# Optimization experiments

Hardware: AMD Instinct MI355X
Metric: run time of the kernel (lower is better)

The kernel has to match this reference:

```python
import jax, jax.numpy as jnp
import numpy as np

HID = 256
SLOTS = 64
K = 2
TAU = 8.0
EPS = 1e-5


def setup_inputs() -> dict:
    key = jax.random.key(0)
    ks = jax.random.split(key, 8)
    B, T = 512, 256
    s = lambda fan_in: 1.0 / np.sqrt(fan_in)
    return {
        "x": jax.random.uniform(ks[0], (B, T, 1), jnp.float32, 0.0, 10.0),
        "W_embed": jax.random.uniform(ks[1], (HID, 1), jnp.float32, -1.0, 1.0),
        "b_embed": jax.random.uniform(ks[2], (HID,), jnp.float32, -1.0, 1.0),
        "W_update": jax.random.uniform(ks[3], (HID, HID), jnp.float32, -s(HID), s(HID)),
        "b_update": jax.random.uniform(ks[4], (HID,), jnp.float32, -s(HID), s(HID)),
        "gamma": jnp.ones((HID,), jnp.float32),
        "beta": jnp.zeros((HID,), jnp.float32),
        "W_out": jax.random.uniform(ks[5], (10, HID), jnp.float32, -s(HID), s(HID)),
        "b_out": jax.random.uniform(ks[6], (10,), jnp.float32, -s(HID), s(HID)),
        "context_strength": jnp.float32(0.2),
    }


def _gaussian_attention(pointer, num_positions):
    # pointer: [B] float. Returns indices [B,5] int32, weights [B,5] float.
    offsets = jnp.arange(-K, K + 1)
    base = jnp.clip(jnp.floor(pointer).astype(jnp.int32), 0, num_positions - 1)
    indices = (base[:, None] + offsets[None, :]) % num_positions
    delta = indices.astype(pointer.dtype) - pointer[:, None]
    weights = jax.nn.softmax(-(delta ** 2) / TAU, axis=1)
    return indices, weights


def reference(x, W_embed, b_embed, W_update, b_update, gamma, beta, W_out, b_out, context_strength):
    B, T, _ = x.shape
    cs = jax.nn.sigmoid(context_strength)

    def step(carry, x_t):
        h, memory, pointer = carry  # [B,H], [B,SLOTS,H], [B]
        inp = jnp.tanh(x_t @ W_embed.T + b_embed)           # [B,H]
        indices, weights = _gaussian_attention(pointer, SLOTS)
        neighborhood = jnp.take_along_axis(memory, indices[:, :, None], axis=1)  # [B,5,H]
        context = jnp.einsum('bk,bkh->bh', weights, neighborhood)
        combined = inp + cs * context
        h = jnp.tanh((combined + h) @ W_update.T + b_update)
        mu = jnp.mean(h, axis=-1, keepdims=True)
        var = jnp.mean((h - mu) ** 2, axis=-1, keepdims=True)
        h = (h - mu) * jax.lax.rsqrt(var + EPS) * gamma + beta
        contribution = weights[:, :, None] * h[:, None, :]   # [B,5,H]
        memory = jax.vmap(lambda m, i, c: m.at[i].add(c))(memory, indices, contribution)
        pointer = (pointer + 1.0) % SLOTS
        return (h, memory, pointer), None

    h0 = jnp.zeros((B, HID), x.dtype)
    mem0 = jnp.zeros((B, SLOTS, HID), x.dtype)
    ptr0 = jnp.zeros((B,), x.dtype)
    (h, _, _), _ = jax.lax.scan(step, (h0, mem0, ptr0), jnp.swapaxes(x, 0, 1))
    return h @ W_out.T + b_out
```

## Files before the change

kernel.cpp:

```cpp
#include <hip/hip_runtime.h>


#define TT 256

typedef __bf16 bf16x8 __attribute__((ext_vector_type(8)));
typedef float  f32x4  __attribute__((ext_vector_type(4)));

__device__ __forceinline__ float fast_tanh(float x) {
    float e = __expf(2.f * x);
    return 1.f - __fdividef(2.f, e + 1.f);
}

template<int CTRL, int RM>
__device__ __forceinline__ float dpp_add(float v) {
    int t = __builtin_amdgcn_update_dpp(0, __float_as_int(v), CTRL, RM, 0xf, true);
    return v + __int_as_float(t);
}
template<int IMM>
__device__ __forceinline__ float swz_add(float v) {
    int t = __builtin_amdgcn_ds_swizzle(__float_as_int(v), IMM);
    return v + __int_as_float(t);
}

#define SMEM_BYTES 136528

__global__ __launch_bounds__(512, 2)
void postnorm_kernel(const float* __restrict__ x,
                     const float* __restrict__ W_embed,
                     const float* __restrict__ b_embed,
                     const float* __restrict__ W_update,
                     const float* __restrict__ b_update,
                     const float* __restrict__ gamma,
                     const float* __restrict__ beta,
                     const float* __restrict__ W_out,
                     const float* __restrict__ b_out,
                     const float* __restrict__ ctx_s,
                     float* __restrict__ out)
{
    extern __shared__ __align__(16) char smem[];
    float*  s_mem  = (float*)(smem);
    float*  s_x    = (float*)(smem + 131072);
    __bf16* s_v    = (__bf16*)(smem + 133120);
    float*  s_red1 = (float*)(smem + 134272);
    float*  s_red2 = (float*)(smem + 134336);
    float*  s_wt   = (float*)(smem + 134400);
    float*  s_oacc = (float*)(smem + 136448);

    const int tid  = threadIdx.x;
    const int wave = tid >> 6;
    const int lane = tid & 63;
    const int bn   = lane & 15;
    const int quad = lane >> 4;
    const int r0   = blockIdx.x * 2;

    const int b     = bn >> 1;
    const int row   = bn & 1;
    const int i_own = wave * 32 + (b >> 2) * 16 + quad * 4 + (b & 3);

    {   f32x4 z = {0.f, 0.f, 0.f, 0.f};
        f32x4* p = (f32x4*)s_mem;
        #pragma unroll
        for (int k = 0; k < 16; ++k) p[tid + k * 512] = z;
    }
    s_x[tid] = x[(r0 + (tid >> 8)) * TT + (tid & 255)];
    if (tid < 20) s_oacc[tid] = 0.f;

    if (tid < 64) {
        float wv[5]; float ssum = 0.f;
        #pragma unroll
        for (int k = 0; k < 5; ++k) {
            int idx = (tid + k - 2) & 63;
            float d = (float)idx - (float)tid;
            wv[k] = expf(-(d * d) * 0.125f);
            ssum += wv[k];
        }
        #pragma unroll
        for (int k = 0; k < 5; ++k) s_wt[tid * 8 + k] = wv[k] / ssum;
    }

    const float we  = W_embed[i_own];
    const float be  = b_embed[i_own];
    const float bu  = b_update[i_own];
    const float gm  = gamma[i_own];
    const float btt = beta[i_own];
    const float csv = 1.f / (1.f + expf(-ctx_s[0]));

    bf16x8 wfa[2][8];
    #pragma unroll
    for (int mt = 0; mt < 2; ++mt) {
        #pragma unroll
        for (int kt = 0; kt < 8; ++kt) {
            const float* wp = W_update + (wave * 32 + mt * 16 + bn) * 256
                                       + kt * 32 + quad * 8;
            f32x4 a = *(const f32x4*)wp;
            f32x4 bb = *(const f32x4*)(wp + 4);
            bf16x8 f;
            f[0] = (__bf16)a[0];  f[1] = (__bf16)a[1];
            f[2] = (__bf16)a[2];  f[3] = (__bf16)a[3];
            f[4] = (__bf16)bb[0]; f[5] = (__bf16)bb[1];
            f[6] = (__bf16)bb[2]; f[7] = (__bf16)bb[3];
            wfa[mt][kt] = f;
        }
    }

    __syncthreads();
    {
        float inp0 = fast_tanh(s_x[row * 256] * we + be);
        s_v[row * 288 + i_own] = (__bf16)inp0;
    }

    float wt0, wt1, wt2, wt3, wt4;
    {   f32x4 wv = *(const f32x4*)(s_wt);
        wt0 = wv[0]; wt1 = wv[1]; wt2 = wv[2]; wt3 = wv[3]; wt4 = s_wt[4];
    }
    f32x4 nw  = *(const f32x4*)(s_wt + 8);
    float nw4 = s_wt[8 + 4];
    float xn  = s_x[row * 256 + 1];
    float nf  = 0.f;
    __syncthreads();

    float hn = 0.f;
    float w0 = 0.f, w1 = 0.f, w2 = 0.f, w3 = 0.f, w4 = 0.f;
    float* mcol = s_mem + (row << 14) + i_own;
    const __bf16* vsrc = s_v + row * 288 + quad * 8;

    #pragma unroll 1
    for (int t = 0; t < TT; ++t) {
        float inp = fast_tanh(xn * we + be);

        f32x4 a0a = {0,0,0,0}, a0b = {0,0,0,0}, a1a = {0,0,0,0}, a1b = {0,0,0,0};
        #pragma unroll
        for (int kt = 0; kt < 4; ++kt) {
            bf16x8 bfr0 = *(const bf16x8*)(vsrc + kt * 32);
            bf16x8 bfr1 = *(const bf16x8*)(vsrc + (kt + 4) * 32);
            a0a = __builtin_amdgcn_mfma_f32_16x16x32_bf16(wfa[0][kt],     bfr0, a0a, 0, 0, 0);
            a1a = __builtin_amdgcn_mfma_f32_16x16x32_bf16(wfa[1][kt],     bfr0, a1a, 0, 0, 0);
            a0b = __builtin_amdgcn_mfma_f32_16x16x32_bf16(wfa[0][kt + 4], bfr1, a0b, 0, 0, 0);
            a1b = __builtin_amdgcn_mfma_f32_16x16x32_bf16(wfa[1][kt + 4], bfr1, a1b, 0, 0, 0);
        }

        f32x4 y0 = a0a + a0b, y1 = a1a + a1b;
        f32x4 ym = (b & 4) ? y1 : y0;
        float yA = (b & 2) ? ym[2] : ym[0];
        float yB = (b & 2) ? ym[3] : ym[1];
        float ysel = (b & 1) ? yB : yA;

        float yt = fast_tanh(ysel + bu);
        float s1 = yt, s2 = yt * yt;
        s1 = dpp_add<0x4E, 0xf>(s1);  s2 = dpp_add<0x4E, 0xf>(s2);
        s1 = swz_add<0x101F>(s1);     s2 = swz_add<0x101F>(s2);
        s1 = swz_add<0x201F>(s1);     s2 = swz_add<0x201F>(s2);
        s1 = swz_add<0x401F>(s1);     s2 = swz_add<0x401F>(s2);
        s1 += __shfl_xor(s1, 32, 64); s2 += __shfl_xor(s2, 32, 64);
        if (lane < 2) {
            s_red1[lane * 8 + wave] = s1;
            s_red2[lane * 8 + wave] = s2;
        }
        __syncthreads();

        f32x4 r1a = *(const f32x4*)(s_red1 + row * 8);
        f32x4 r1b = *(const f32x4*)(s_red1 + row * 8 + 4);
        f32x4 r2a = *(const f32x4*)(s_red2 + row * 8);
        f32x4 r2b = *(const f32x4*)(s_red2 + row * 8 + 4);
        float S1 = ((r1a[0] + r1a[1]) + (r1a[2] + r1a[3]))
                 + ((r1b[0] + r1b[1]) + (r1b[2] + r1b[3]));
        float S2 = ((r2a[0] + r2a[1]) + (r2a[2] + r2a[3]))
                 + ((r2b[0] + r2b[1]) + (r2b[2] + r2b[3]));
        float mu   = S1 * (1.f / 256.f);
        float var  = S2 * (1.f / 256.f) - mu * mu;
        float rstd = rsqrtf(var + 1e-5f);
        hn = (yt - mu) * rstd * gm + btt;

        w0 += wt0 * hn; w1 += wt1 * hn; w2 += wt2 * hn;
        w3 += wt3 * hn; w4 += wt4 * hn;

        mcol[((t - 2) & 63) << 8] = w0;
        w0 = w1; w1 = w2; w2 = w3; w3 = w4; w4 = nf;
        float ctx = ((nw[0] * w0 + nw[1] * w1) + (nw[2] * w2 + nw[3] * w3))
                  + nw4 * w4;
        float v = inp + csv * ctx + hn;
        s_v[row * 288 + i_own] = (__bf16)v;
        wt0 = nw[0]; wt1 = nw[1]; wt2 = nw[2]; wt3 = nw[3]; wt4 = nw4;

        nf  = mcol[((t + 4) & 63) << 8];
        {   const float* wp = s_wt + ((t + 2) & 63) * 8;
            nw  = *(const f32x4*)wp;
            nw4 = wp[4];
        }
        xn  = s_x[row * 256 + ((t + 2) & 255)];
        __syncthreads();
    }

    s_x[row * 256 + i_own] = hn;
    __syncthreads();
    {
        const int n = tid >> 8, i = tid & 255;
        float h = s_x[tid];
        #pragma unroll
        for (int o = 0; o < 10; ++o) {
            float p = h * W_out[o * 256 + i];
            #pragma unroll
            for (int m = 32; m >= 1; m >>= 1) p += __shfl_xor(p, m, 64);
            if (lane == 0) atomicAdd(&s_oacc[n * 10 + o], p);
        }
    }
    __syncthreads();
    if (tid < 20) {
        int nn = tid / 10, o = tid % 10;
        out[(r0 + nn) * 10 + o] = s_oacc[tid] + b_out[o];
    }
}

extern "C" void kernel_launch(void* const* d_in, const int* in_sizes, int n_in,
                              void* d_out, int out_size, void* d_ws, size_t ws_size,
                              hipStream_t stream) {
    const float* x    = (const float*)d_in[0];
    const float* W_e  = (const float*)d_in[1];
    const float* b_e  = (const float*)d_in[2];
    const float* W_u  = (const float*)d_in[3];
    const float* b_u  = (const float*)d_in[4];
    const float* gmm  = (const float*)d_in[5];
    const float* bta  = (const float*)d_in[6];
    const float* W_o  = (const float*)d_in[7];
    const float* b_o  = (const float*)d_in[8];
    const float* cst  = (const float*)d_in[9];
    float* out = (float*)d_out;

    (void)hipFuncSetAttribute(reinterpret_cast<const void*>(postnorm_kernel),
                              hipFuncAttributeMaxDynamicSharedMemorySize,
                              SMEM_BYTES);

    postnorm_kernel<<<dim3(256), dim3(512), SMEM_BYTES, stream>>>(
        x, W_e, b_e, W_u, b_u, gmm, bta, W_o, b_o, cst, out);
}
```

Baseline: 310.7 us.

## Fold LayerNorm into the matmul to drop one barrier per timestep

The recurrence is restructured algebraically. The raw tanh output (scaled by gamma) goes into the MFMA as a second operand column, and the LayerNorm mean and rstd are applied afterward as scalar corrections, using a precomputed W·gamma vector (yG) and a DPP exchange between paired lanes. This removes the mid-step barrier between the reduction and the next matvec. The reduction and s_v buffers are double-buffered, so each step needs only one __syncthreads, at the cost of doubling the N columns used in the MFMA and some added bf16 rounding error on the unnormalized values.

```diff
diff --git a/kernel.cpp b/kernel.cpp
--- a/kernel.cpp
+++ b/kernel.cpp
@@ -21,8 +21,12 @@
     int t = __builtin_amdgcn_ds_swizzle(__float_as_int(v), IMM);
     return v + __int_as_float(t);
 }
-
-#define SMEM_BYTES 136528
+__device__ __forceinline__ float dpp_xor2_mov(float v) {
+    int t = __builtin_amdgcn_update_dpp(0, __float_as_int(v), 0x4E, 0xf, 0xf, true);
+    return __int_as_float(t);
+}
+
+#define SMEM_BYTES 139856
 
 __global__ __launch_bounds__(512, 2)
 void postnorm_kernel(const float* __restrict__ x,
@@ -41,10 +45,10 @@
     float*  s_mem  = (float*)(smem);
     float*  s_x    = (float*)(smem + 131072);
     __bf16* s_v    = (__bf16*)(smem + 133120);
-    float*  s_red1 = (float*)(smem + 134272);
-    float*  s_red2 = (float*)(smem + 134336);
-    float*  s_wt   = (float*)(smem + 134400);
-    float*  s_oacc = (float*)(smem + 136448);
+    float*  s_red1 = (float*)(smem + 137472);
+    float*  s_red2 = (float*)(smem + 137600);
+    float*  s_wt   = (float*)(smem + 137728);
+    float*  s_oacc = (float*)(smem + 139776);
 
     const int tid  = threadIdx.x;
     const int wave = tid >> 6;
@@ -53,9 +57,12 @@
     const int quad = lane >> 4;
     const int r0   = blockIdx.x * 2;
 
-    const int b     = bn >> 1;
-    const int row   = bn & 1;
-    const int i_own = wave * 32 + (b >> 2) * 16 + quad * 4 + (b & 3);
+    const int row  = bn & 1;
+    const int pq   = (bn >> 1) & 1;
+    const int rep  = bn >> 2;
+    const int mt   = rep >> 1;
+    const int rsel = (rep & 1) * 2 + pq;
+    const int i_own = wave * 32 + mt * 16 + quad * 4 + rsel;
 
     {   f32x4 z = {0.f, 0.f, 0.f, 0.f};
         f32x4* p = (f32x4*)s_mem;
@@ -63,6 +70,7 @@
         for (int k = 0; k < 16; ++k) p[tid + k * 512] = z;
     }
     s_x[tid] = x[(r0 + (tid >> 8)) * TT + (tid & 255)];
+    if (tid < 64) ((float*)(smem + 137472))[tid] = 0.f;
     if (tid < 20) s_oacc[tid] = 0.f;
 
     if (tid < 64) {
@@ -87,10 +95,10 @@
 
     bf16x8 wfa[2][8];
     #pragma unroll
-    for (int mt = 0; mt < 2; ++mt) {
+    for (int mtt = 0; mtt < 2; ++mtt) {
         #pragma unroll
         for (int kt = 0; kt < 8; ++kt) {
-            const float* wp = W_update + (wave * 32 + mt * 16 + bn) * 256
+            const float* wp = W_update + (wave * 32 + mtt * 16 + bn) * 256
                                        + kt * 32 + quad * 8;
             f32x4 a = *(const f32x4*)wp;
             f32x4 bb = *(const f32x4*)(wp + 4);
@@ -99,35 +107,17 @@
             f[2] = (__bf16)a[2];  f[3] = (__bf16)a[3];
             f[4] = (__bf16)bb[0]; f[5] = (__bf16)bb[1];
             f[6] = (__bf16)bb[2]; f[7] = (__bf16)bb[3];
-            wfa[mt][kt] = f;
-        }
-    }
-
-    __syncthreads();
-    {
-        float inp0 = fast_tanh(s_x[row * 256] * we + be);
-        s_v[row * 288 + i_own] = (__bf16)inp0;
-    }
-
-    float wt0, wt1, wt2, wt3, wt4;
-    {   f32x4 wv = *(const f32x4*)(s_wt);
-        wt0 = wv[0]; wt1 = wv[1]; wt2 = wv[2]; wt3 = wv[3]; wt4 = s_wt[4];
-    }
-    f32x4 nw  = *(const f32x4*)(s_wt + 8);
-    float nw4 = s_wt[8 + 4];
-    float xn  = s_x[row * 256 + 1];
-    float nf  = 0.f;
-    __syncthreads();
-
-    float hn = 0.f;
-    float w0 = 0.f, w1 = 0.f, w2 = 0.f, w3 = 0.f, w4 = 0.f;
-    float* mcol = s_mem + (row << 14) + i_own;
-    const __bf16* vsrc = s_v + row * 288 + quad * 8;
-
-    #pragma unroll 1
-    for (int t = 0; t < TT; ++t) {
-        float inp = fast_tanh(xn * we + be);
-
+            wfa[mtt][kt] = f;
+        }
+    }
+
+    s_v[row * 272 + i_own]       = (__bf16)gm;
+    s_v[(row + 2) * 272 + i_own] = (__bf16)gm;
+    __syncthreads();
+
+    float yG;
+    {
+        const __bf16* vsrc = s_v + (bn & 3) * 272 + quad * 8;
         f32x4 a0a = {0,0,0,0}, a0b = {0,0,0,0}, a1a = {0,0,0,0}, a1b = {0,0,0,0};
         #pragma unroll
         for (int kt = 0; kt < 4; ++kt) {
@@ -138,14 +128,76 @@
             a0b = __builtin_amdgcn_mfma_f32_16x16x32_bf16(wfa[0][kt + 4], bfr1, a0b, 0, 0, 0);
             a1b = __builtin_amdgcn_mfma_f32_16x16x32_bf16(wfa[1][kt + 4], bfr1, a1b, 0, 0, 0);
         }
-
         f32x4 y0 = a0a + a0b, y1 = a1a + a1b;
-        f32x4 ym = (b & 4) ? y1 : y0;
-        float yA = (b & 2) ? ym[2] : ym[0];
-        float yB = (b & 2) ? ym[3] : ym[1];
-        float ysel = (b & 1) ? yB : yA;
-
-        float yt = fast_tanh(ysel + bu);
+        f32x4 ym = mt ? y1 : y0;
+        float pl = (rep & 1) ? ym[2] : ym[0];
+        float ph = (rep & 1) ? ym[3] : ym[1];
+        yG = pq ? ph : pl;
+    }
+    __syncthreads();
+
+    {
+        float inp0 = fast_tanh(s_x[row * 256] * we + be);
+        s_v[row * 272 + i_own]       = (__bf16)inp0;
+        s_v[(row + 2) * 272 + i_own] = (__bf16)0.f;
+    }
+
+    float wm0 = s_wt[63*8+0], wm1 = s_wt[63*8+1], wm2 = s_wt[63*8+2],
+          wm3 = s_wt[63*8+3], wm4 = s_wt[63*8+4];
+    float wc0 = s_wt[0], wc1 = s_wt[1], wc2 = s_wt[2],
+          wc3 = s_wt[3], wc4 = s_wt[4];
+    float wp0 = s_wt[8+0], wp1 = s_wt[8+1], wp2 = s_wt[8+2],
+          wp3 = s_wt[8+3], wp4 = s_wt[8+4];
+    float u0 = 0.f, u1 = 0.f, u2 = 0.f, u3 = 0.f, u4 = 0.f, u5 = 0.f;
+    float yt_prev = 0.f, C_cur = 1.f;
+    float* mcol = s_mem + (row << 14) + i_own;
+    float nf = mcol[3 << 8];
+    float xn = s_x[row * 256 + 1];
+    float hn = 0.f;
+    __syncthreads();
+
+    #pragma unroll 1
+    for (int t = 0; t < TT; ++t) {
+        const int rb = t & 1, wb = rb ^ 1;
+
+        const float* rp1 = s_red1 + (wb * 2 + row) * 8;
+        const float* rp2 = s_red2 + (wb * 2 + row) * 8;
+        f32x4 r1a = *(const f32x4*)rp1, r1b = *(const f32x4*)(rp1 + 4);
+        f32x4 r2a = *(const f32x4*)rp2, r2b = *(const f32x4*)(rp2 + 4);
+
+        const __bf16* vsrc = s_v + (rb * 4 + (bn & 3)) * 272 + quad * 8;
+        f32x4 a0a = {0,0,0,0}, a0b = {0,0,0,0}, a1a = {0,0,0,0}, a1b = {0,0,0,0};
+        #pragma unroll
+        for (int kt = 0; kt < 4; ++kt) {
+            bf16x8 bfr0 = *(const bf16x8*)(vsrc + kt * 32);
+            bf16x8 bfr1 = *(const bf16x8*)(vsrc + (kt + 4) * 32);
+            a0a = __builtin_amdgcn_mfma_f32_16x16x32_bf16(wfa[0][kt],     bfr0, a0a, 0, 0, 0);
+            a1a = __builtin_amdgcn_mfma_f32_16x16x32_bf16(wfa[1][kt],     bfr0, a1a, 0, 0, 0);
+            a0b = __builtin_amdgcn_mfma_f32_16x16x32_bf16(wfa[0][kt + 4], bfr1, a0b, 0, 0, 0);
+            a1b = __builtin_amdgcn_mfma_f32_16x16x32_bf16(wfa[1][kt + 4], bfr1, a1b, 0, 0, 0);
+        }
+
+        float S1 = ((r1a[0]+r1a[1])+(r1a[2]+r1a[3])) + ((r1b[0]+r1b[1])+(r1b[2]+r1b[3]));
+        float S2 = ((r2a[0]+r2a[1])+(r2a[2]+r2a[3])) + ((r2b[0]+r2b[1])+(r2b[2]+r2b[3]));
+        float mu   = S1 * (1.f / 256.f);
+        float var  = S2 * (1.f / 256.f) - mu * mu;
+        float rstd = rsqrtf(var + 1e-5f);
+        const float m0 = (t == 0) ? 0.f : 1.f;
+        float aC = rstd * C_cur * m0;
+        float bC = -mu * aC;
+
+        f32x4 y0 = a0a + a0b, y1 = a1a + a1b;
+        f32x4 ym = mt ? y1 : y0;
+        float pl = (rep & 1) ? ym[2] : ym[0];
+        float ph = (rep & 1) ? ym[3] : ym[1];
+        float own  = pq ? ph : pl;
+        float give = pq ? pl : ph;
+        float recv = dpp_xor2_mov(give);
+        float yP = pq ? recv : own;
+        float yQ = pq ? own  : recv;
+        float y  = yP + aC * yQ + bC * yG;
+
+        float yt = fast_tanh(y + bu);
         float s1 = yt, s2 = yt * yt;
         s1 = dpp_add<0x4E, 0xf>(s1);  s2 = dpp_add<0x4E, 0xf>(s2);
         s1 = swz_add<0x101F>(s1);     s2 = swz_add<0x101F>(s2);
@@ -153,45 +205,51 @@
         s1 = swz_add<0x401F>(s1);     s2 = swz_add<0x401F>(s2);
         s1 += __shfl_xor(s1, 32, 64); s2 += __shfl_xor(s2, 32, 64);
         if (lane < 2) {
-            s_red1[lane * 8 + wave] = s1;
-            s_red2[lane * 8 + wave] = s2;
-        }
+            s_red1[(rb * 2 + lane) * 8 + wave] = s1;
+            s_red2[(rb * 2 + lane) * 8 + wave] = s2;
+        }
+
+        hn = m0 * ((yt_prev - mu) * rstd * gm + btt);
+        u0 += wm0 * hn; u1 += wm1 * hn; u2 += wm2 * hn;
+        u3 += wm3 * hn; u4 += wm4 * hn;
+        mcol[((t - 3) & 63) << 8] = u0;
+        u0 = u1; u1 = u2; u2 = u3; u3 = u4; u4 = u5; u5 = nf;
+
+        float ctxB = ((wp0 * u1 + wp1 * u2) + (wp2 * u3 + wp3 * u4)) + wp4 * u5;
+        float wd   = (wp0 * wc1 + wp1 * wc2) + (wp2 * wc3 + wp3 * wc4);
+        float Cn   = 1.f + csv * wd;
+        float inp  = fast_tanh(xn * we + be);
+        float vP   = inp + csv * ctxB + Cn * btt;
+        float vQ   = gm * yt;
+        __bf16* svw = s_v + wb * 1088;
+        svw[row * 272 + i_own]       = (__bf16)vP;
+        svw[(row + 2) * 272 + i_own] = (__bf16)vQ;
+
+        C_cur = Cn;  yt_prev = yt;
+        wm0 = wc0; wm1 = wc1; wm2 = wc2; wm3 = wc3; wm4 = wc4;
+        wc0 = wp0; wc1 = wp1; wc2 = wp2; wc3 = wp3; wc4 = wp4;
+        {   const float* wrow = s_wt + ((t + 2) & 63) * 8;
+            f32x4 wn = *(const f32x4*)wrow;
+            wp0 = wn[0]; wp1 = wn[1]; wp2 = wn[2]; wp3 = wn[3]; wp4 = wrow[4];
+        }
+        nf = mcol[((t + 4) & 63) << 8];
+        xn = s_x[row * 256 + ((t + 2) & 255)];
         __syncthreads();
-
-        f32x4 r1a = *(const f32x4*)(s_red1 + row * 8);
-        f32x4 r1b = *(const f32x4*)(s_red1 + row * 8 + 4);
-        f32x4 r2a = *(const f32x4*)(s_red2 + row * 8);
-        f32x4 r2b = *(const f32x4*)(s_red2 + row * 8 + 4);
-        float S1 = ((r1a[0] + r1a[1]) + (r1a[2] + r1a[3]))
-                 + ((r1b[0] + r1b[1]) + (r1b[2] + r1b[3]));
-        float S2 = ((r2a[0] + r2a[1]) + (r2a[2] + r2a[3]))
-                 + ((r2b[0] + r2b[1]) + (r2b[2] + r2b[3]));
+    }
+
+    {
+        const float* rp1 = s_red1 + (1 * 2 + row) * 8;
+        const float* rp2 = s_red2 + (1 * 2 + row) * 8;
+        f32x4 r1a = *(const f32x4*)rp1, r1b = *(const f32x4*)(rp1 + 4);
+        f32x4 r2a = *(const f32x4*)rp2, r2b = *(const f32x4*)(rp2 + 4);
+        float S1 = ((r1a[0]+r1a[1])+(r1a[2]+r1a[3])) + ((r1b[0]+r1b[1])+(r1b[2]+r1b[3]));
+        float S2 = ((r2a[0]+r2a[1])+(r2a[2]+r2a[3])) + ((r2b[0]+r2b[1])+(r2b[2]+r2b[3]));
         float mu   = S1 * (1.f / 256.f);
         float var  = S2 * (1.f / 256.f) - mu * mu;
         float rstd = rsqrtf(var + 1e-5f);
-        hn = (yt - mu) * rstd * gm + btt;
-
-        w0 += wt0 * hn; w1 += wt1 * hn; w2 += wt2 * hn;
-        w3 += wt3 * hn; w4 += wt4 * hn;
-
-        mcol[((t - 2) & 63) << 8] = w0;
-        w0 = w1; w1 = w2; w2 = w3; w3 = w4; w4 = nf;
-        float ctx = ((nw[0] * w0 + nw[1] * w1) + (nw[2] * w2 + nw[3] * w3))
-                  + nw4 * w4;
-        float v = inp + csv * ctx + hn;
-        s_v[row * 288 + i_own] = (__bf16)v;
-        wt0 = nw[0]; wt1 = nw[1]; wt2 = nw[2]; wt3 = nw[3]; wt4 = nw4;
-
-        nf  = mcol[((t + 4) & 63) << 8];
-        {   const float* wp = s_wt + ((t + 2) & 63) * 8;
-            nw  = *(const f32x4*)wp;
-            nw4 = wp[4];
-        }
-        xn  = s_x[row * 256 + ((t + 2) & 255)];
-        __syncthreads();
-    }
-
-    s_x[row * 256 + i_own] = hn;
+        float hfin = (yt_prev - mu) * rstd * gm + btt;
+        s_x[row * 256 + i_own] = hfin;
+    }
     __syncthreads();
     {
         const int n = tid >> 8, i = tid & 255;
```

Measured after the change: 330.0 us. 1.06x slower.
